# Optimization experiments

Measured on AMD Instinct MI355X. Metric: run time of the kernel, lower is better.

## Reference

```python
import jax, jax.numpy as jnp
import numpy as np

B, T = 2, 512
D, H, DFF = 1024, 16, 4096
V, CSL = 32000, 16
NL, NDL = 4, 2
MAXLEN = 1024
DH = D // H


def generate_ar_mask(L, csl):
    m = np.zeros((2 * L, 2 * L), dtype=bool)
    for i in range(L):
        m[:i] = True
        m[L + (i // csl) * csl: L + i] = True
    return jnp.asarray(m)


def generate_block_ntp_mask(L, csl):
    m = np.zeros((2 * L, 2 * L), dtype=bool)
    for c in range(L // csl):
        if c - 1 >= 0:
            m[:(c - 1) * csl] = True
        m[L + c * csl: L + (c + 1) * csl] = True
    return jnp.asarray(m)


def layernorm(x, g, b, eps=1e-5):
    mu = x.mean(-1, keepdims=True)
    var = x.var(-1, keepdims=True)
    return (x - mu) / jnp.sqrt(var + eps) * g + b


def block(x, mask, p):
    ln1g, ln1b, wqkv, bqkv, wo, bo, ln2g, ln2b, w1, b1, w2, b2 = p
    h = layernorm(x, ln1g, ln1b)
    qkv = h @ wqkv + bqkv                       # [B,S,3D]
    q, k, v = jnp.split(qkv, 3, axis=-1)
    bs, S, _ = x.shape
    q = q.reshape(bs, S, H, DH).transpose(0, 2, 1, 3)
    k = k.reshape(bs, S, H, DH).transpose(0, 2, 1, 3)
    v = v.reshape(bs, S, H, DH).transpose(0, 2, 1, 3)
    scores = jnp.einsum('bhqd,bhkd->bhqk', q, k) / jnp.sqrt(jnp.asarray(DH, x.dtype))
    scores = jnp.where(mask, scores, jnp.asarray(-1e9, x.dtype))
    attn = jax.nn.softmax(scores, axis=-1)
    o = jnp.einsum('bhqk,bhkd->bhqd', attn, v)
    o = o.transpose(0, 2, 1, 3).reshape(bs, S, D)
    x = x + (o @ wo + bo)
    h = layernorm(x, ln2g, ln2b)
    return x + (jax.nn.gelu(h @ w1 + b1, approximate=False) @ w2 + b2)


def setup_inputs():
    key = jax.random.key(0)
    ks = jax.random.split(key, 6)

    def pstack(k, n):
        kk = jax.random.split(k, 4)
        return dict(
            ln1g=jnp.ones((n, D)), ln1b=jnp.zeros((n, D)),
            wqkv=0.02 * jax.random.normal(kk[0], (n, D, 3 * D)), bqkv=jnp.zeros((n, 3 * D)),
            wo=0.02 * jax.random.normal(kk[1], (n, D, D)), bo=jnp.zeros((n, D)),
            ln2g=jnp.ones((n, D)), ln2b=jnp.zeros((n, D)),
            w1=0.02 * jax.random.normal(kk[2], (n, D, DFF)), b1=jnp.zeros((n, DFF)),
            w2=0.02 * jax.random.normal(kk[3], (n, DFF, D)), b2=jnp.zeros((n, D)))

    body = pstack(ks[0], NL)
    dec = pstack(ks[1], NDL)
    inp = {
        'tok_ids': jax.random.randint(ks[2], (B, T), 0, V),
        'tok_emb': 0.02 * jax.random.normal(ks[3], (V, D)),
        'pos_emb': 0.02 * jax.random.normal(ks[4], (MAXLEN, D)),
        'mask_tokens': 0.02 * jax.random.normal(ks[5], (1, CSL, D)),
    }
    for kname, vv in body.items():
        inp['b_' + kname] = vv
    for kname, vv in dec.items():
        inp['d_' + kname] = vv
    return inp


def reference(tok_ids, tok_emb, pos_emb, mask_tokens,
              b_ln1g, b_ln1b, b_wqkv, b_bqkv, b_wo, b_bo, b_ln2g, b_ln2b, b_w1, b_b1, b_w2, b_b2,
              d_ln1g, d_ln1b, d_wqkv, d_bqkv, d_wo, d_bo, d_ln2g, d_ln2b, d_w1, d_b1, d_w2, d_b2):
    Bq, Tq = tok_ids.shape
    pos = jnp.tile(jnp.arange(Tq), 2)            # pos ids repeated for both halves
    emb_pos = pos_emb[pos]                       # [2T, D], broadcast over batch
    mask_ids = jnp.tile(mask_tokens, (Bq, Tq // CSL, 1))
    x = jnp.concatenate([tok_emb[tok_ids], mask_ids], axis=1) + emb_pos[None]

    body_mask = generate_block_ntp_mask(Tq, CSL)
    bp = (b_ln1g, b_ln1b, b_wqkv, b_bqkv, b_wo, b_bo, b_ln2g, b_ln2b, b_w1, b_b1, b_w2, b_b2)
    for i in range(NL):
        x = block(x, body_mask, tuple(p[i] for p in bp))

    ar_mask = generate_ar_mask(Tq, CSL)
    dp = (d_ln1g, d_ln1b, d_wqkv, d_bqkv, d_wo, d_bo, d_ln2g, d_ln2b, d_w1, d_b1, d_w2, d_b2)
    for i in range(NDL):
        x = block(x, ar_mask, tuple(p[i] for p in dp))

    logits = (x @ tok_emb.T)[:, Tq + 1:, :]      # [B, T-1, V]
    tgt = tok_ids[:, :-1].reshape(-1)
    logits = logits.reshape(-1, V)
    logp = jax.nn.log_softmax(logits, axis=-1)
    loss = -jnp.take_along_axis(logp, tgt[:, None], axis=1).mean()
    return loss
```

## Files before the change

kernel.cpp:

```cpp
#include <hip/hip_runtime.h>
#include <hip/hip_bf16.h>
#include <math.h>

#define DD   1024
#define HHN  16
#define DHD  64
#define DFFN 4096
#define VV   32000
#define BBN  2
#define TTN  512
#define SSN  1024
#define NRN  2048

typedef __attribute__((ext_vector_type(8))) short short8;
typedef __attribute__((ext_vector_type(4))) float f32x4;

enum : long {
    LSTR    = 12582912,
    OFF_QKV = 0,
    OFF_WO  = 3145728,
    OFF_W1  = 4194304,
    OFF_W2  = 8388608
};

struct P24 { const float* p[24]; };

__device__ __forceinline__ unsigned short f2bf(float f) {
    __hip_bfloat16 h = __float2bfloat16(f);
    return __builtin_bit_cast(unsigned short, h);
}
__device__ __forceinline__ float bf2f(unsigned short u) {
    return __bfloat162float(__builtin_bit_cast(__hip_bfloat16, u));
}

__device__ __forceinline__ void glds16(const void* g, void* l) {
    __builtin_amdgcn_global_load_lds(
        (const __attribute__((address_space(1))) void*)g,
        (__attribute__((address_space(3))) void*)l,
        16, 0, 0);
}

__device__ __forceinline__ float blockReduceSum(float v) {
    __shared__ float sh[4];
    #pragma unroll
    for (int o = 1; o < 64; o <<= 1) v += __shfl_xor(v, o, 64);
    int lane = threadIdx.x & 63, wv = threadIdx.x >> 6;
    __syncthreads();
    if (lane == 0) sh[wv] = v;
    __syncthreads();
    return sh[0] + sh[1] + sh[2] + sh[3];
}

__global__ __launch_bounds__(256) void embed_k(const int* __restrict__ tok,
                                               const float* __restrict__ temb,
                                               const float* __restrict__ pemb,
                                               const float* __restrict__ mtok,
                                               float* __restrict__ x) {
    int row = blockIdx.x;
    int b = row >> 10, s = row & 1023;
    int d = threadIdx.x * 4;
    const float* src;
    const float* pe;
    if (s < TTN) {
        int id = tok[b * TTN + s];
        src = temb + (size_t)id * DD + d;
        pe  = pemb + (size_t)s * DD + d;
    } else {
        int sm = s - TTN;
        src = mtok + (size_t)(sm & 15) * DD + d;
        pe  = pemb + (size_t)sm * DD + d;
    }
    float4 v = *(const float4*)src;
    float4 p = *(const float4*)pe;
    v.x += p.x; v.y += p.y; v.z += p.z; v.w += p.w;
    *(float4*)(x + (size_t)row * DD + d) = v;
}

__global__ __launch_bounds__(256) void ln_k(const float* __restrict__ x,
                                            const float* __restrict__ g,
                                            const float* __restrict__ b,
                                            unsigned short* __restrict__ out) {
    int row = blockIdx.x;
    int d = threadIdx.x * 4;
    const float4 v = *(const float4*)(x + (size_t)row * DD + d);
    float s  = v.x + v.y + v.z + v.w;
    float ss = v.x * v.x + v.y * v.y + v.z * v.z + v.w * v.w;
    s  = blockReduceSum(s);
    ss = blockReduceSum(ss);
    float mu  = s * (1.0f / DD);
    float var = ss * (1.0f / DD) - mu * mu;
    float inv = rsqrtf(var + 1e-5f);
    const float4 gg = *(const float4*)(g + d);
    const float4 bb = *(const float4*)(b + d);
    ushort4 o;
    o.x = f2bf((v.x - mu) * inv * gg.x + bb.x);
    o.y = f2bf((v.y - mu) * inv * gg.y + bb.y);
    o.z = f2bf((v.z - mu) * inv * gg.z + bb.z);
    o.w = f2bf((v.w - mu) * inv * gg.w + bb.w);
    *(ushort4*)(out + (size_t)row * DD + d) = o;
}

__global__ __launch_bounds__(256) void convTall_k(P24 wp, unsigned short* __restrict__ wbf) {
    __shared__ __align__(16) unsigned short tile[64][72];
    int id = blockIdx.x;
    int seg, base, K, N;
    long woff;
    if (id < 4608)       { seg = 0; base = 0;     K = DD;   N = 3 * DD; woff = OFF_QKV; }
    else if (id < 6144)  { seg = 1; base = 4608;  K = DD;   N = DD;     woff = OFF_WO;  }
    else if (id < 12288) { seg = 2; base = 6144;  K = DD;   N = DFFN;   woff = OFF_W1;  }
    else                 { seg = 3; base = 12288; K = DFFN; N = DD;     woff = OFF_W2;  }
    const int rid = id - base;
    const int tpl = (K / 64) * (N / 64);
    const int lz = rid / tpl, t2 = rid % tpl;
    const int nt = N / 64;
    const int n0 = (t2 % nt) * 64, k0 = (t2 / nt) * 64;
    const float* w = wp.p[seg * 6 + lz];
    unsigned short* wt = wbf + (size_t)lz * LSTR + woff;

    const int t = threadIdx.x;
    {
        const int kr = t >> 2, nc = (t & 3) * 16;
        const float* src = w + (size_t)(k0 + kr) * N + n0 + nc;
        float4 f0 = ((const float4*)src)[0];
        float4 f1 = ((const float4*)src)[1];
        float4 f2 = ((const float4*)src)[2];
        float4 f3 = ((const float4*)src)[3];
        __align__(16) unsigned short tmp[16];
        tmp[0]=f2bf(f0.x); tmp[1]=f2bf(f0.y); tmp[2]=f2bf(f0.z); tmp[3]=f2bf(f0.w);
        tmp[4]=f2bf(f1.x); tmp[5]=f2bf(f1.y); tmp[6]=f2bf(f1.z); tmp[7]=f2bf(f1.w);
        tmp[8]=f2bf(f2.x); tmp[9]=f2bf(f2.y); tmp[10]=f2bf(f2.z); tmp[11]=f2bf(f2.w);
        tmp[12]=f2bf(f3.x); tmp[13]=f2bf(f3.y); tmp[14]=f2bf(f3.z); tmp[15]=f2bf(f3.w);
        *(int4*)&tile[kr][nc]     = *(const int4*)&tmp[0];
        *(int4*)&tile[kr][nc + 8] = *(const int4*)&tmp[8];
    }
    __syncthreads();
    {
        const int nr = t >> 2, kc = (t & 3) * 16;
        __align__(16) unsigned short tmp[16];
        #pragma unroll
        for (int i = 0; i < 16; i++) tmp[i] = tile[kc + i][nr];
        unsigned short* d2 = wt + (size_t)(n0 + nr) * K + k0 + kc;
        *(int4*)d2       = *(const int4*)&tmp[0];
        *(int4*)(d2 + 8) = *(const int4*)&tmp[8];
    }
}

__global__ __launch_bounds__(256) void conv_k(const float* __restrict__ w,
                                              unsigned short* __restrict__ o, long n) {
    long i = ((long)blockIdx.x * 256 + threadIdx.x) * 8;
    if (i >= n) return;
    float4 a = *(const float4*)(w + i);
    float4 b = *(const float4*)(w + i + 4);
    __align__(16) unsigned short tmp[8];
    tmp[0] = f2bf(a.x); tmp[1] = f2bf(a.y); tmp[2] = f2bf(a.z); tmp[3] = f2bf(a.w);
    tmp[4] = f2bf(b.x); tmp[5] = f2bf(b.y); tmp[6] = f2bf(b.z); tmp[7] = f2bf(b.w);
    *(int4*)(o + i) = *(const int4*)tmp;
}

__global__ __launch_bounds__(256, 2) void flash_k(
    const unsigned short* __restrict__ qkvb,
    unsigned short* __restrict__ o,
    int mtype) {
    __shared__ __align__(16) unsigned short Qs[128][72];
    __shared__ __align__(16) unsigned short Ks[64][72];
    __shared__ __align__(16) unsigned short Vs[64][72];
    __shared__ __align__(16) unsigned short Ps[128][72];
    __shared__ float vcol[64];

    const int blk = blockIdx.x;
    const int bh = blk >> 3, qt = blk & 7;
    const int b = bh >> 4, h = bh & 15;
    const int t = threadIdx.x;
    const int lane = t & 63;
    const int w = t >> 6;
    const int fr = lane & 15;
    const int g8 = (lane >> 4) * 8;
    const int g4 = (lane >> 4) * 4;

    {
        const int r = t >> 1, c0 = (t & 1) * 32;
        const unsigned short* src =
            qkvb + (size_t)(b * SSN + qt * 128 + r) * 3072 + h * 64 + c0;
        *(int4*)&Qs[r][c0]      = *(const int4*)(src);
        *(int4*)&Qs[r][c0 + 8]  = *(const int4*)(src + 8);
        *(int4*)&Qs[r][c0 + 16] = *(const int4*)(src + 16);
        *(int4*)&Qs[r][c0 + 24] = *(const int4*)(src + 24);
    }
    __syncthreads();
    short8 aq[2][2];
    #pragma unroll
    for (int m = 0; m < 2; m++)
        #pragma unroll
        for (int kk = 0; kk < 2; kk++)
            aq[m][kk] = *(const short8*)&Qs[w * 32 + m * 16 + fr][kk * 32 + g8];

    float mrun[2][4], lrun[2][4];
    f32x4 accO[2][4] = {};
    #pragma unroll
    for (int m = 0; m < 2; m++)
        #pragma unroll
        for (int j = 0; j < 4; j++) { mrun[m][j] = -1e30f; lrun[m][j] = 0.f; }

    float vacc[16];
    #pragma unroll
    for (int j = 0; j < 16; j++) vacc[j] = 0.f;

    const unsigned short* kbase = qkvb + (size_t)(b * SSN) * 3072 + DD + h * 64;
    const unsigned short* vbase = qkvb + (size_t)(b * SSN) * 3072 + 2 * DD + h * 64;
    const int d0 = w * 16;

    for (int kt = 0; kt < 16; kt++) {
        __syncthreads();
        {
            const int r = t >> 2, c0 = (t & 3) * 16;
            const unsigned short* src = kbase + (size_t)(kt * 64 + r) * 3072 + c0;
            *(int4*)&Ks[r][c0]     = *(const int4*)(src);
            *(int4*)&Ks[r][c0 + 8] = *(const int4*)(src + 8);
        }
        {
            const unsigned short* src = vbase + (size_t)(kt * 64 + lane) * 3072 + d0;
            int4 q0 = *(const int4*)(src);
            int4 q1 = *(const int4*)(src + 8);
            const unsigned short* u = (const unsigned short*)&q0;
            #pragma unroll
            for (int j = 0; j < 8; j++) {
                Vs[d0 + j][lane] = u[j];
                vacc[j] += bf2f(u[j]);
            }
            const unsigned short* u2 = (const unsigned short*)&q1;
            #pragma unroll
            for (int j = 0; j < 8; j++) {
                Vs[d0 + 8 + j][lane] = u2[j];
                vacc[8 + j] += bf2f(u2[j]);
            }
        }
        __syncthreads();

        short8 bk[4][2];
        #pragma unroll
        for (int n = 0; n < 4; n++)
            #pragma unroll
            for (int kk = 0; kk < 2; kk++)
                bk[n][kk] = *(const short8*)&Ks[n * 16 + fr][kk * 32 + g8];

        #pragma unroll
        for (int m = 0; m < 2; m++) {
            f32x4 a2[4] = {};
            #pragma unroll
            for (int n = 0; n < 4; n++) {
                a2[n] = __builtin_amdgcn_mfma_f32_16x16x32_bf16(aq[m][0], bk[n][0], a2[n], 0, 0, 0);
                a2[n] = __builtin_amdgcn_mfma_f32_16x16x32_bf16(aq[m][1], bk[n][1], a2[n], 0, 0, 0);
            }
            #pragma unroll
            for (int j = 0; j < 4; j++) {
                float tm = fmaxf(fmaxf(a2[0][j], a2[1][j]), fmaxf(a2[2][j], a2[3][j]));
                tm *= 0.125f;
                #pragma unroll
                for (int o2 = 1; o2 < 16; o2 <<= 1) tm = fmaxf(tm, __shfl_xor(tm, o2, 64));
                const float mn = fmaxf(mrun[m][j], tm);
                const float alpha = __expf(mrun[m][j] - mn);
                mrun[m][j] = mn;
                float rs = 0.f;
                #pragma unroll
                for (int n = 0; n < 4; n++) {
                    float pv = __expf(a2[n][j] * 0.125f - mn);
                    rs += pv;
                    Ps[w * 32 + m * 16 + g4 + j][n * 16 + fr] = f2bf(pv);
                }
                #pragma unroll
                for (int o2 = 1; o2 < 16; o2 <<= 1) rs += __shfl_xor(rs, o2, 64);
                lrun[m][j] = lrun[m][j] * alpha + rs;
                #pragma unroll
                for (int nd = 0; nd < 4; nd++) accO[m][nd][j] *= alpha;
            }
        }
        #pragma unroll
        for (int kk = 0; kk < 2; kk++) {
            short8 pa0 = *(const short8*)&Ps[w * 32 + fr][kk * 32 + g8];
            short8 pa1 = *(const short8*)&Ps[w * 32 + 16 + fr][kk * 32 + g8];
            #pragma unroll
            for (int nd = 0; nd < 4; nd++) {
                short8 vb = *(const short8*)&Vs[nd * 16 + fr][kk * 32 + g8];
                accO[0][nd] = __builtin_amdgcn_mfma_f32_16x16x32_bf16(pa0, vb, accO[0][nd], 0, 0, 0);
                accO[1][nd] = __builtin_amdgcn_mfma_f32_16x16x32_bf16(pa1, vb, accO[1][nd], 0, 0, 0);
            }
        }
    }

    #pragma unroll
    for (int j = 0; j < 16; j++) {
        float vs = vacc[j];
        #pragma unroll
        for (int o2 = 1; o2 < 64; o2 <<= 1) vs += __shfl_xor(vs, o2, 64);
        if (lane == j) vcol[d0 + j] = vs;
    }
    __syncthreads();

    #pragma unroll
    for (int m = 0; m < 2; m++)
        #pragma unroll
        for (int nd = 0; nd < 4; nd++)
            #pragma unroll
            for (int j = 0; j < 4; j++) {
                const int row = qt * 128 + w * 32 + m * 16 + g4 + j;
                const int col = nd * 16 + fr;
                bool uni;
                if (mtype == 0) uni = (row >= 480 && row < 512);
                else            uni = (row == 511) || (row >= 512 && (row & 15) == 15);
                float val;
                if (uni) val = vcol[col] * (1.0f / 1024.0f);
                else     val = accO[m][nd][j] / lrun[m][j];
                o[(size_t)(b * SSN + row) * DD + h * 64 + col] = f2bf(val);
            }
}

template <bool DOLN>
__global__ __launch_bounds__(256) void rln_k(const float* __restrict__ pp,
                                             const float* __restrict__ bias,
                                             float* __restrict__ x,
                                             const float* __restrict__ g,
                                             const float* __restrict__ b,
                                             unsigned short* __restrict__ xb) {
    const int row = blockIdx.x;
    const int d = threadIdx.x * 4;
    const size_t off = (size_t)row * DD + d;
    float4 v = *(const float4*)(x + off);
    #pragma unroll
    for (int sl = 0; sl < 4; sl++) {
        float4 p = *(const float4*)(pp + (size_t)sl * NRN * DD + off);
        v.x += p.x; v.y += p.y; v.z += p.z; v.w += p.w;
    }
    const float4 bv = *(const float4*)(bias + d);
    v.x += bv.x; v.y += bv.y; v.z += bv.z; v.w += bv.w;
    *(float4*)(x + off) = v;
    if (DOLN) {
        float s  = v.x + v.y + v.z + v.w;
        float ss = v.x * v.x + v.y * v.y + v.z * v.z + v.w * v.w;
        s  = blockReduceSum(s);
        ss = blockReduceSum(ss);
        float mu  = s * (1.0f / DD);
        float var = ss * (1.0f / DD) - mu * mu;
        float inv = rsqrtf(var + 1e-5f);
        const float4 gg = *(const float4*)(g + d);
        const float4 bb = *(const float4*)(b + d);
        ushort4 ov;
        ov.x = f2bf((v.x - mu) * inv * gg.x + bb.x);
        ov.y = f2bf((v.y - mu) * inv * gg.y + bb.y);
        ov.z = f2bf((v.z - mu) * inv * gg.z + bb.z);
        ov.w = f2bf((v.w - mu) * inv * gg.w + bb.w);
        *(ushort4*)(xb + off) = ov;
    }
}

__global__ __launch_bounds__(256) void gather_xl_k(const float* __restrict__ x,
                                                   unsigned short* __restrict__ xl) {
    int r = blockIdx.x;
    int d = threadIdx.x * 4;
    ushort4 o = {0, 0, 0, 0};
    if (r < 1022) {
        int b = r / 511, i = r % 511;
        float4 v = *(const float4*)(x + (size_t)(b * SSN + 513 + i) * DD + d);
        o.x = f2bf(v.x); o.y = f2bf(v.y); o.z = f2bf(v.z); o.w = f2bf(v.w);
    }
    *(ushort4*)(xl + (size_t)r * DD + d) = o;
}

__global__ __launch_bounds__(256) void loss_row_k(const unsigned short* __restrict__ logits,
                                                  const int* __restrict__ tok,
                                                  float* __restrict__ rowloss) {
    int r = blockIdx.x;
    const unsigned short* p = logits + (size_t)r * VV;
    int t = threadIdx.x;
    float mx = -1e30f, s = 0.f;
    for (int c = t; c < VV / 8; c += 256) {
        int4 q = *(const int4*)(p + c * 8);
        const unsigned short* u = (const unsigned short*)&q;
        #pragma unroll
        for (int j = 0; j < 8; j++) {
            float v = bf2f(u[j]);
            if (v > mx) { s *= __expf(mx - v); mx = v; }
            s += __expf(v - mx);
        }
    }
    #pragma unroll
    for (int o2 = 1; o2 < 64; o2 <<= 1) {
        float om = __shfl_xor(mx, o2, 64);
        float os = __shfl_xor(s, o2, 64);
        float m2 = fmaxf(mx, om);
        s = s * __expf(mx - m2) + os * __expf(om - m2);
        mx = m2;
    }
    __shared__ float shm[4], shs[4];
    int lane = t & 63, wv = t >> 6;
    if (lane == 0) { shm[wv] = mx; shs[wv] = s; }
    __syncthreads();
    if (t == 0) {
        float M = fmaxf(fmaxf(shm[0], shm[1]), fmaxf(shm[2], shm[3]));
        float S = shs[0] * __expf(shm[0] - M) + shs[1] * __expf(shm[1] - M)
                + shs[2] * __expf(shm[2] - M) + shs[3] * __expf(shm[3] - M);
        int b = r / 511, i2 = r % 511;
        int tgt = tok[b * TTN + i2];
        rowloss[r] = (logf(S) + M) - bf2f(p[tgt]);
    }
}

__global__ __launch_bounds__(256) void loss_final_k(const float* __restrict__ rowloss,
                                                    float* __restrict__ out) {
    int t = threadIdx.x;
    float s = 0.f;
    for (int i = t; i < 1022; i += 256) s += rowloss[i];
    s = blockReduceSum(s);
    if (t == 0) out[0] = s * (1.0f / 1022.0f);
}

template <int EPI, int KSPLIT>
__global__ __launch_bounds__(256) void gemm_k(
    const unsigned short* __restrict__ A, long lda,
    const unsigned short* __restrict__ Bt, long ldb,
    void* __restrict__ Cp, long ldc,
    const float* __restrict__ bias,
    int MT, int K, long kstr) {
    __shared__ __align__(16) unsigned short As[2][128][32];
    __shared__ __align__(16) unsigned short Bs[2][128][32];

    const int nwg = gridDim.x;
    const int q = nwg >> 3, r = nwg & 7;
    const int xcd = blockIdx.x & 7, lin = blockIdx.x >> 3;
    const int wg = (xcd < r ? xcd * (q + 1) : r * (q + 1) + (xcd - r) * q) + lin;
    const int tiles = nwg / KSPLIT;
    const int ks = wg / tiles;
    const int rem = wg % tiles;
    const int brow = (rem % MT) * 128;
    const int bcol = (rem / MT) * 128;
    const int Kl = K / KSPLIT;

    const int t = threadIdx.x;
    const int lane = t & 63;
    const int w = t >> 6;
    const int fr = lane & 15;
    const int g8 = (lane >> 4) * 8;

    const int sr = w * 32 + (lane >> 2);
    const int sc = (lane & 3) * 8;
    const unsigned short* aP0 = A + (size_t)(brow + sr) * lda + ks * Kl + sc;
    const unsigned short* aP1 = aP0 + (size_t)16 * lda;
    const unsigned short* bP0 = Bt + (size_t)(bcol + sr) * ldb + ks * Kl + sc;
    const unsigned short* bP1 = bP0 + (size_t)16 * ldb;

    f32x4 acc[4][4] = {};
    const int nsteps = Kl >> 5;

    glds16(aP0, &As[0][w * 32][0]);
    glds16(aP1, &As[0][w * 32 + 16][0]);
    glds16(bP0, &Bs[0][w * 32][0]);
    glds16(bP1, &Bs[0][w * 32 + 16][0]);
    aP0 += 32; aP1 += 32; bP0 += 32; bP1 += 32;
    asm volatile("s_waitcnt vmcnt(0)");
    __syncthreads();

    int cur = 0;
    for (int s2 = 1; s2 < nsteps; ++s2) {
        const int nb = cur ^ 1;
        glds16(aP0, &As[nb][w * 32][0]);
        glds16(aP1, &As[nb][w * 32 + 16][0]);
        glds16(bP0, &Bs[nb][w * 32][0]);
        glds16(bP1, &Bs[nb][w * 32 + 16][0]);
        aP0 += 32; aP1 += 32; bP0 += 32; bP1 += 32;

        short8 af[4], bf[4];
        #pragma unroll
        for (int m = 0; m < 4; m++)
            af[m] = *(const short8*)&As[cur][(w >> 1) * 64 + m * 16 + fr][g8];
        #pragma unroll
        for (int n = 0; n < 4; n++)
            bf[n] = *(const short8*)&Bs[cur][(w & 1) * 64 + n * 16 + fr][g8];
        #pragma unroll
        for (int m = 0; m < 4; m++)
            #pragma unroll
            for (int n = 0; n < 4; n++)
                acc[m][n] = __builtin_amdgcn_mfma_f32_16x16x32_bf16(af[m], bf[n], acc[m][n], 0, 0, 0);
        __syncthreads();
        cur = nb;
    }
    {
        short8 af[4], bf[4];
        #pragma unroll
        for (int m = 0; m < 4; m++)
            af[m] = *(const short8*)&As[cur][(w >> 1) * 64 + m * 16 + fr][g8];
        #pragma unroll
        for (int n = 0; n < 4; n++)
            bf[n] = *(const short8*)&Bs[cur][(w & 1) * 64 + n * 16 + fr][g8];
        #pragma unroll
        for (int m = 0; m < 4; m++)
            #pragma unroll
            for (int n = 0; n < 4; n++)
                acc[m][n] = __builtin_amdgcn_mfma_f32_16x16x32_bf16(af[m], bf[n], acc[m][n], 0, 0, 0);
    }

    const int wr = (w >> 1) * 64;
    const int wc = (w & 1) * 64;
    const int g4 = (lane >> 4) * 4;
    #pragma unroll
    for (int n = 0; n < 4; n++) {
        const int col = bcol + wc + n * 16 + fr;
        const float bv = bias ? bias[col] : 0.f;
        #pragma unroll
        for (int m = 0; m < 4; m++) {
            #pragma unroll
            for (int j = 0; j < 4; j++) {
                const int row = brow + wr + m * 16 + g4 + j;
                float v = acc[m][n][j] + bv;
                const size_t ci = (size_t)row * ldc + col;
                if (EPI == 0) {
                    ((float*)Cp)[ci] = v;
                } else if (EPI == 1) {
                    ((unsigned short*)Cp)[ci] = f2bf(v);
                } else if (EPI == 2) {
                    float gl = 0.5f * v * (1.0f + erff(v * 0.70710678118654752f));
                    ((unsigned short*)Cp)[ci] = f2bf(gl);
                } else if (EPI == 3) {
                    ((float*)Cp)[ci] += v;
                } else {
                    ((float*)Cp)[(size_t)ks * kstr + ci] = v;
                }
            }
        }
    }
}

extern "C" void kernel_launch(void* const* d_in, const int* in_sizes, int n_in,
                              void* d_out, int out_size, void* d_ws, size_t ws_size,
                              hipStream_t stream) {
    const int*   tok  = (const int*)d_in[0];
    const float* temb = (const float*)d_in[1];
    const float* pemb = (const float*)d_in[2];
    const float* mtok = (const float*)d_in[3];
    const float* W[24];
    for (int i = 0; i < 24; i++) W[i] = (const float*)d_in[4 + i];

    char* ws = (char*)d_ws;
    float*          x      = (float*)(ws + 0);
    unsigned short* xb     = (unsigned short*)(ws + 8388608);
    unsigned short* qkvb   = (unsigned short*)(ws + 12582912);
    unsigned short* o      = (unsigned short*)(ws + 25165824);
    unsigned short* g      = (unsigned short*)(ws + 29360128);
    float*          pp     = (float*)(ws + 46137344);
    unsigned short* wbf    = (unsigned short*)(ws + 79691776);
    unsigned short* tembb  = (unsigned short*)(ws + 79691776);
    unsigned short* logits = (unsigned short*)(ws + 145227776);
    unsigned short* xl     = (unsigned short*)(ws + 230686720);
    float*          rowloss= (float*)(ws + 232783872);

    P24 wp;
    for (int l = 0; l < 6; l++) {
        const int grp = (l < 4) ? 0 : 1;
        const int li  = (l < 4) ? l : l - 4;
        const float* const* P = W + grp * 12;
        wp.p[0 + l]  = P[2]  + (size_t)li * DD * 3 * DD;
        wp.p[6 + l]  = P[4]  + (size_t)li * DD * DD;
        wp.p[12 + l] = P[8]  + (size_t)li * DD * DFFN;
        wp.p[18 + l] = P[10] + (size_t)li * DFFN * DD;
    }
    convTall_k<<<18432, 256, 0, stream>>>(wp, wbf);

    embed_k<<<NRN, 256, 0, stream>>>(tok, temb, pemb, mtok, x);

    for (int l = 0; l < 6; l++) {
        const int grp = (l < 4) ? 0 : 1;
        const int li  = (l < 4) ? l : l - 4;
        const float* const* P = W + grp * 12;
        const float* ln1g = P[0] + (size_t)li * DD;
        const float* ln1b = P[1] + (size_t)li * DD;
        const float* bqkv = P[3] + (size_t)li * 3 * DD;
        const float* bo   = P[5] + (size_t)li * DD;
        const float* ln2g = P[6] + (size_t)li * DD;
        const float* ln2b = P[7] + (size_t)li * DD;
        const float* b1   = P[9] + (size_t)li * DFFN;
        const float* b2   = P[11] + (size_t)li * DD;
        unsigned short* wl = wbf + (size_t)l * LSTR;

        if (l == 0) ln_k<<<NRN, 256, 0, stream>>>(x, ln1g, ln1b, xb);
        gemm_k<1, 1><<<16 * 24, 256, 0, stream>>>(xb, DD, wl + OFF_QKV, DD,
                                                  qkvb, 3 * DD, bqkv, 16, DD, 0);
        flash_k<<<256, 256, 0, stream>>>(qkvb, o, grp);
        gemm_k<3, 1><<<16 * 8, 256, 0, stream>>>(o, DD, wl + OFF_WO, DD,
                                                 x, DD, bo, 16, DD, 0);

        ln_k<<<NRN, 256, 0, stream>>>(x, ln2g, ln2b, xb);
        gemm_k<2, 1><<<16 * 32, 256, 0, stream>>>(xb, DD, wl + OFF_W1, DD,
                                                  g, DFFN, b1, 16, DD, 0);
        gemm_k<4, 4><<<16 * 8 * 4, 256, 0, stream>>>(g, DFFN, wl + OFF_W2, DFFN,
                                                     pp, DD, nullptr, 16, DFFN,
                                                     (long)NRN * DD);
        if (l < 5) {
            const int l2 = l + 1;
            const int grp2 = (l2 < 4) ? 0 : 1;
            const int li2  = (l2 < 4) ? l2 : l2 - 4;
            const float* const* P2 = W + grp2 * 12;
            rln_k<true><<<NRN, 256, 0, stream>>>(pp, b2, x,
                                                 P2[0] + (size_t)li2 * DD,
                                                 P2[1] + (size_t)li2 * DD, xb);
        } else {
            rln_k<false><<<NRN, 256, 0, stream>>>(pp, b2, x, nullptr, nullptr, nullptr);
        }
    }

    gather_xl_k<<<1024, 256, 0, stream>>>(x, xl);
    conv_k<<<16000, 256, 0, stream>>>(temb, tembb, (long)VV * DD);
    gemm_k<1, 1><<<8 * 250, 256, 0, stream>>>(xl, DD, tembb, DD,
                                              logits, VV, nullptr, 8, DD, 0);
    loss_row_k<<<1022, 256, 0, stream>>>(logits, tok, rowloss);
    loss_final_k<<<1, 256, 0, stream>>>(rowloss, (float*)d_out);
}
```

Baseline: 1.504 ms.

## Fuse logits GEMM with partial log-sum-exp and merge weight prep with embedding

Replaces the vocab-logits GEMM plus row-loss pass with a GEMM whose epilogue emits per-64-column (max, sumexp) partials and picks out the target logit, so the 1022x32000 bf16 logits tensor is never written or re-read. A small second kernel then merges the 500 partials per row. The weight transpose/convert kernel and the embedding kernel are also merged into one launch, with the transpose now staging fp32 in shared memory and converting on read. The cost is a heavier GEMM epilogue with shuffles and exps, and more shared memory in the prep kernel.

```diff
diff --git a/kernel.cpp b/kernel.cpp
--- a/kernel.cpp
+++ b/kernel.cpp
@@ -51,29 +51,73 @@
     return sh[0] + sh[1] + sh[2] + sh[3];
 }
 
-__global__ __launch_bounds__(256) void embed_k(const int* __restrict__ tok,
-                                               const float* __restrict__ temb,
-                                               const float* __restrict__ pemb,
-                                               const float* __restrict__ mtok,
-                                               float* __restrict__ x) {
-    int row = blockIdx.x;
-    int b = row >> 10, s = row & 1023;
-    int d = threadIdx.x * 4;
-    const float* src;
-    const float* pe;
-    if (s < TTN) {
-        int id = tok[b * TTN + s];
-        src = temb + (size_t)id * DD + d;
-        pe  = pemb + (size_t)s * DD + d;
+__global__ __launch_bounds__(256) void prep_k(P24 wp, unsigned short* __restrict__ wbf,
+                                              const int* __restrict__ tok,
+                                              const float* __restrict__ temb,
+                                              const float* __restrict__ pemb,
+                                              const float* __restrict__ mtok,
+                                              float* __restrict__ x) {
+    __shared__ __align__(16) float Lf[64][68];
+    const int id = blockIdx.x;
+    const int t = threadIdx.x;
+
+    if (id < 18432) {
+        int seg, base, K, N;
+        long woff;
+        if (id < 4608)       { seg = 0; base = 0;     K = DD;   N = 3 * DD; woff = OFF_QKV; }
+        else if (id < 6144)  { seg = 1; base = 4608;  K = DD;   N = DD;     woff = OFF_WO;  }
+        else if (id < 12288) { seg = 2; base = 6144;  K = DD;   N = DFFN;   woff = OFF_W1;  }
+        else                 { seg = 3; base = 12288; K = DFFN; N = DD;     woff = OFF_W2;  }
+        const int rid = id - base;
+        const int tpl = (K / 64) * (N / 64);
+        const int lz = rid / tpl, t2 = rid % tpl;
+        const int nt = N / 64;
+        const int n0 = (t2 % nt) * 64, k0 = (t2 / nt) * 64;
+        const float* w = wp.p[seg * 6 + lz];
+        unsigned short* wt = wbf + (size_t)lz * LSTR + woff;
+
+        {
+            const int kr = t >> 2, nc = (t & 3) * 16;
+            const float* src = w + (size_t)(k0 + kr) * N + n0 + nc;
+            float4 f0 = ((const float4*)src)[0];
+            float4 f1 = ((const float4*)src)[1];
+            float4 f2 = ((const float4*)src)[2];
+            float4 f3 = ((const float4*)src)[3];
+            *(float4*)&Lf[kr][nc]      = f0;
+            *(float4*)&Lf[kr][nc + 4]  = f1;
+            *(float4*)&Lf[kr][nc + 8]  = f2;
+            *(float4*)&Lf[kr][nc + 12] = f3;
+        }
+        __syncthreads();
+        {
+            const int nr = t & 63, kc = (t >> 6) * 16;
+            __align__(16) unsigned short tmp[16];
+            #pragma unroll
+            for (int i = 0; i < 16; i++) tmp[i] = f2bf(Lf[kc + i][nr]);
+            unsigned short* d2 = wt + (size_t)(n0 + nr) * K + k0 + kc;
+            *(int4*)d2       = *(const int4*)&tmp[0];
+            *(int4*)(d2 + 8) = *(const int4*)&tmp[8];
+        }
     } else {
-        int sm = s - TTN;
-        src = mtok + (size_t)(sm & 15) * DD + d;
-        pe  = pemb + (size_t)sm * DD + d;
-    }
-    float4 v = *(const float4*)src;
-    float4 p = *(const float4*)pe;
-    v.x += p.x; v.y += p.y; v.z += p.z; v.w += p.w;
-    *(float4*)(x + (size_t)row * DD + d) = v;
+        const int row = id - 18432;
+        const int b = row >> 10, s = row & 1023;
+        const int d = t * 4;
+        const float* src;
+        const float* pe;
+        if (s < TTN) {
+            int tid2 = tok[b * TTN + s];
+            src = temb + (size_t)tid2 * DD + d;
+            pe  = pemb + (size_t)s * DD + d;
+        } else {
+            int sm = s - TTN;
+            src = mtok + (size_t)(sm & 15) * DD + d;
+            pe  = pemb + (size_t)sm * DD + d;
+        }
+        float4 v = *(const float4*)src;
+        float4 p = *(const float4*)pe;
+        v.x += p.x; v.y += p.y; v.z += p.z; v.w += p.w;
+        *(float4*)(x + (size_t)row * DD + d) = v;
+    }
 }
 
 __global__ __launch_bounds__(256) void ln_k(const float* __restrict__ x,
@@ -100,51 +144,6 @@
     *(ushort4*)(out + (size_t)row * DD + d) = o;
 }
 
-__global__ __launch_bounds__(256) void convTall_k(P24 wp, unsigned short* __restrict__ wbf) {
-    __shared__ __align__(16) unsigned short tile[64][72];
-    int id = blockIdx.x;
-    int seg, base, K, N;
-    long woff;
-    if (id < 4608)       { seg = 0; base = 0;     K = DD;   N = 3 * DD; woff = OFF_QKV; }
-    else if (id < 6144)  { seg = 1; base = 4608;  K = DD;   N = DD;     woff = OFF_WO;  }
-    else if (id < 12288) { seg = 2; base = 6144;  K = DD;   N = DFFN;   woff = OFF_W1;  }
-    else                 { seg = 3; base = 12288; K = DFFN; N = DD;     woff = OFF_W2;  }
-    const int rid = id - base;
-    const int tpl = (K / 64) * (N / 64);
-    const int lz = rid / tpl, t2 = rid % tpl;
-    const int nt = N / 64;
-    const int n0 = (t2 % nt) * 64, k0 = (t2 / nt) * 64;
-    const float* w = wp.p[seg * 6 + lz];
-    unsigned short* wt = wbf + (size_t)lz * LSTR + woff;
-
-    const int t = threadIdx.x;
-    {
-        const int kr = t >> 2, nc = (t & 3) * 16;
-        const float* src = w + (size_t)(k0 + kr) * N + n0 + nc;
-        float4 f0 = ((const float4*)src)[0];
-        float4 f1 = ((const float4*)src)[1];
-        float4 f2 = ((const float4*)src)[2];
-        float4 f3 = ((const float4*)src)[3];
-        __align__(16) unsigned short tmp[16];
-        tmp[0]=f2bf(f0.x); tmp[1]=f2bf(f0.y); tmp[2]=f2bf(f0.z); tmp[3]=f2bf(f0.w);
-        tmp[4]=f2bf(f1.x); tmp[5]=f2bf(f1.y); tmp[6]=f2bf(f1.z); tmp[7]=f2bf(f1.w);
-        tmp[8]=f2bf(f2.x); tmp[9]=f2bf(f2.y); tmp[10]=f2bf(f2.z); tmp[11]=f2bf(f2.w);
-        tmp[12]=f2bf(f3.x); tmp[13]=f2bf(f3.y); tmp[14]=f2bf(f3.z); tmp[15]=f2bf(f3.w);
-        *(int4*)&tile[kr][nc]     = *(const int4*)&tmp[0];
-        *(int4*)&tile[kr][nc + 8] = *(const int4*)&tmp[8];
-    }
-    __syncthreads();
-    {
-        const int nr = t >> 2, kc = (t & 3) * 16;
-        __align__(16) unsigned short tmp[16];
-        #pragma unroll
-        for (int i = 0; i < 16; i++) tmp[i] = tile[kc + i][nr];
-        unsigned short* d2 = wt + (size_t)(n0 + nr) * K + k0 + kc;
-        *(int4*)d2       = *(const int4*)&tmp[0];
-        *(int4*)(d2 + 8) = *(const int4*)&tmp[8];
-    }
-}
-
 __global__ __launch_bounds__(256) void conv_k(const float* __restrict__ w,
                                               unsigned short* __restrict__ o, long n) {
     long i = ((long)blockIdx.x * 256 + threadIdx.x) * 8;
@@ -365,22 +364,17 @@
     *(ushort4*)(xl + (size_t)r * DD + d) = o;
 }
 
-__global__ __launch_bounds__(256) void loss_row_k(const unsigned short* __restrict__ logits,
-                                                  const int* __restrict__ tok,
-                                                  float* __restrict__ rowloss) {
-    int r = blockIdx.x;
-    const unsigned short* p = logits + (size_t)r * VV;
-    int t = threadIdx.x;
+__global__ __launch_bounds__(256) void loss_row2_k(const float2* __restrict__ part,
+                                                   const float* __restrict__ tgtlog,
+                                                   float* __restrict__ rowloss) {
+    const int r = blockIdx.x;
+    const int t = threadIdx.x;
     float mx = -1e30f, s = 0.f;
-    for (int c = t; c < VV / 8; c += 256) {
-        int4 q = *(const int4*)(p + c * 8);
-        const unsigned short* u = (const unsigned short*)&q;
-        #pragma unroll
-        for (int j = 0; j < 8; j++) {
-            float v = bf2f(u[j]);
-            if (v > mx) { s *= __expf(mx - v); mx = v; }
-            s += __expf(v - mx);
-        }
+    for (int i = t; i < 500; i += 256) {
+        float2 p = part[(size_t)r * 500 + i];
+        float m2 = fmaxf(mx, p.x);
+        s = s * __expf(mx - m2) + p.y * __expf(p.x - m2);
+        mx = m2;
     }
     #pragma unroll
     for (int o2 = 1; o2 < 64; o2 <<= 1) {
@@ -398,9 +392,7 @@
         float M = fmaxf(fmaxf(shm[0], shm[1]), fmaxf(shm[2], shm[3]));
         float S = shs[0] * __expf(shm[0] - M) + shs[1] * __expf(shm[1] - M)
                 + shs[2] * __expf(shm[2] - M) + shs[3] * __expf(shm[3] - M);
-        int b = r / 511, i2 = r % 511;
-        int tgt = tok[b * TTN + i2];
-        rowloss[r] = (logf(S) + M) - bf2f(p[tgt]);
+        rowloss[r] = (logf(S) + M) - tgtlog[r];
     }
 }
 
@@ -528,6 +520,118 @@
     }
 }
 
+__global__ __launch_bounds__(256) void gemm_lse_k(
+    const unsigned short* __restrict__ A,
+    const unsigned short* __restrict__ Bt,
+    float2* __restrict__ part,
+    float* __restrict__ tgtlog,
+    const int* __restrict__ tok) {
+    __shared__ __align__(16) unsigned short As[2][128][32];
+    __shared__ __align__(16) unsigned short Bs[2][128][32];
+
+    const int nwg = gridDim.x;
+    const int q = nwg >> 3, r = nwg & 7;
+    const int xcd = blockIdx.x & 7, lin = blockIdx.x >> 3;
+    const int wg = (xcd < r ? xcd * (q + 1) : r * (q + 1) + (xcd - r) * q) + lin;
+    const int MT = 8;
+    const int brow = (wg % MT) * 128;
+    const int bcol = (wg / MT) * 128;
+
+    const int t = threadIdx.x;
+    const int lane = t & 63;
+    const int w = t >> 6;
+    const int fr = lane & 15;
+    const int g8 = (lane >> 4) * 8;
+
+    const int sr = w * 32 + (lane >> 2);
+    const int sc = (lane & 3) * 8;
+    const unsigned short* aP0 = A + (size_t)(brow + sr) * DD + sc;
+    const unsigned short* aP1 = aP0 + (size_t)16 * DD;
+    const unsigned short* bP0 = Bt + (size_t)(bcol + sr) * DD + sc;
+    const unsigned short* bP1 = bP0 + (size_t)16 * DD;
+
+    f32x4 acc[4][4] = {};
+
+    glds16(aP0, &As[0][w * 32][0]);
+    glds16(aP1, &As[0][w * 32 + 16][0]);
+    glds16(bP0, &Bs[0][w * 32][0]);
+    glds16(bP1, &Bs[0][w * 32 + 16][0]);
+    aP0 += 32; aP1 += 32; bP0 += 32; bP1 += 32;
+    asm volatile("s_waitcnt vmcnt(0)");
+    __syncthreads();
+
+    int cur = 0;
+    for (int s2 = 1; s2 < 32; ++s2) {
+        const int nb = cur ^ 1;
+        glds16(aP0, &As[nb][w * 32][0]);
+        glds16(aP1, &As[nb][w * 32 + 16][0]);
+        glds16(bP0, &Bs[nb][w * 32][0]);
+        glds16(bP1, &Bs[nb][w * 32 + 16][0]);
+        aP0 += 32; aP1 += 32; bP0 += 32; bP1 += 32;
+
+        short8 af[4], bf[4];
+        #pragma unroll
+        for (int m = 0; m < 4; m++)
+            af[m] = *(const short8*)&As[cur][(w >> 1) * 64 + m * 16 + fr][g8];
+        #pragma unroll
+        for (int n = 0; n < 4; n++)
+            bf[n] = *(const short8*)&Bs[cur][(w & 1) * 64 + n * 16 + fr][g8];
+        #pragma unroll
+        for (int m = 0; m < 4; m++)
+            #pragma unroll
+            for (int n = 0; n < 4; n++)
+                acc[m][n] = __builtin_amdgcn_mfma_f32_16x16x32_bf16(af[m], bf[n], acc[m][n], 0, 0, 0);
+        __syncthreads();
+        cur = nb;
+    }
+    {
+        short8 af[4], bf[4];
+        #pragma unroll
+        for (int m = 0; m < 4; m++)
+            af[m] = *(const short8*)&As[cur][(w >> 1) * 64 + m * 16 + fr][g8];
+        #pragma unroll
+        for (int n = 0; n < 4; n++)
+            bf[n] = *(const short8*)&Bs[cur][(w & 1) * 64 + n * 16 + fr][g8];
+        #pragma unroll
+        for (int m = 0; m < 4; m++)
+            #pragma unroll
+            for (int n = 0; n < 4; n++)
+                acc[m][n] = __builtin_amdgcn_mfma_f32_16x16x32_bf16(af[m], bf[n], acc[m][n], 0, 0, 0);
+    }
+
+    const int wr = (w >> 1) * 64;
+    const int wc = (w & 1) * 64;
+    const int g4 = (lane >> 4) * 4;
+    const int ct2 = (bcol >> 7) * 2 + (w & 1);
+    #pragma unroll
+    for (int m = 0; m < 4; m++) {
+        #pragma unroll
+        for (int j = 0; j < 4; j++) {
+            const int grow = brow + wr + m * 16 + g4 + j;
+            const float v0 = acc[m][0][j], v1 = acc[m][1][j];
+            const float v2 = acc[m][2][j], v3 = acc[m][3][j];
+            float mx = fmaxf(fmaxf(v0, v1), fmaxf(v2, v3));
+            #pragma unroll
+            for (int o2 = 1; o2 < 16; o2 <<= 1) mx = fmaxf(mx, __shfl_xor(mx, o2, 64));
+            float s = __expf(v0 - mx) + __expf(v1 - mx) + __expf(v2 - mx) + __expf(v3 - mx);
+            #pragma unroll
+            for (int o2 = 1; o2 < 16; o2 <<= 1) s += __shfl_xor(s, o2, 64);
+            if (fr == 0) {
+                float2 p; p.x = mx; p.y = s;
+                part[(size_t)grow * 500 + ct2] = p;
+            }
+            int tgtc = -1;
+            if (grow < 511) tgtc = tok[grow];
+            else if (grow >= 511 && grow < 1022) tgtc = tok[512 + grow - 511];
+            const int cl = tgtc - (bcol + wc);
+            if (tgtc >= 0 && cl >= 0 && cl < 64 && (cl & 15) == fr) {
+                const float vv[4] = {v0, v1, v2, v3};
+                tgtlog[grow] = vv[cl >> 4];
+            }
+        }
+    }
+}
+
 extern "C" void kernel_launch(void* const* d_in, const int* in_sizes, int n_in,
                               void* d_out, int out_size, void* d_ws, size_t ws_size,
                               hipStream_t stream) {
@@ -547,7 +651,8 @@
     float*          pp     = (float*)(ws + 46137344);
     unsigned short* wbf    = (unsigned short*)(ws + 79691776);
     unsigned short* tembb  = (unsigned short*)(ws + 79691776);
-    unsigned short* logits = (unsigned short*)(ws + 145227776);
+    float2*         part   = (float2*)(ws + 145227776);
+    float*          tgtlog = (float*)(ws + 149327872);
     unsigned short* xl     = (unsigned short*)(ws + 230686720);
     float*          rowloss= (float*)(ws + 232783872);
 
@@ -561,9 +666,7 @@
         wp.p[12 + l] = P[8]  + (size_t)li * DD * DFFN;
         wp.p[18 + l] = P[10] + (size_t)li * DFFN * DD;
     }
-    convTall_k<<<18432, 256, 0, stream>>>(wp, wbf);
-
-    embed_k<<<NRN, 256, 0, stream>>>(tok, temb, pemb, mtok, x);
+    prep_k<<<18432 + 2048, 256, 0, stream>>>(wp, wbf, tok, temb, pemb, mtok, x);
 
     for (int l = 0; l < 6; l++) {
         const int grp = (l < 4) ? 0 : 1;
@@ -607,8 +710,7 @@
 
     gather_xl_k<<<1024, 256, 0, stream>>>(x, xl);
     conv_k<<<16000, 256, 0, stream>>>(temb, tembb, (long)VV * DD);
-    gemm_k<1, 1><<<8 * 250, 256, 0, stream>>>(xl, DD, tembb, DD,
-                                              logits, VV, nullptr, 8, DD, 0);
-    loss_row_k<<<1022, 256, 0, stream>>>(logits, tok, rowloss);
+    gemm_lse_k<<<2000, 256, 0, stream>>>(xl, tembb, part, tgtlog, tok);
+    loss_row2_k<<<1022, 256, 0, stream>>>(part, tgtlog, rowloss);
     loss_final_k<<<1, 256, 0, stream>>>(rowloss, (float*)d_out);
 }
```

After: 1.501 ms. About the same (-0.2%).
